# Kernel optimization log

Measured on AMD Instinct MI355X. Metric: run time of the kernel, lower is better.

The kernel has to match this reference:

```python
import jax, jax.numpy as jnp
import numpy as np

DIM = 256
NUM_EXPERTS = 16
EXPERT_HIDDEN = 128
ROUTER_HIDDEN = 64
N_TOKENS = 32768


def setup_inputs() -> dict:
    key = jax.random.key(0)
    ks = jax.random.split(key, 9)
    s = lambda fan_in: 1.0 / np.sqrt(fan_in)
    x = jax.random.normal(ks[0], (N_TOKENS, DIM), dtype=jnp.float32)
    # Router params (Linear(DIM,64) -> ReLU -> Linear(64,E))
    r_w1 = jax.random.uniform(ks[1], (DIM, ROUTER_HIDDEN), jnp.float32, -s(DIM), s(DIM))
    r_b1 = jax.random.uniform(ks[2], (ROUTER_HIDDEN,), jnp.float32, -s(DIM), s(DIM))
    r_w2 = jax.random.uniform(ks[3], (ROUTER_HIDDEN, NUM_EXPERTS), jnp.float32, -s(ROUTER_HIDDEN), s(ROUTER_HIDDEN))
    r_b2 = jax.random.uniform(ks[4], (NUM_EXPERTS,), jnp.float32, -s(ROUTER_HIDDEN), s(ROUTER_HIDDEN))
    # Expert params, stacked over experts: Linear(DIM,128) -> Tanh -> Linear(128,DIM)
    e_w1 = jax.random.uniform(ks[5], (NUM_EXPERTS, DIM, EXPERT_HIDDEN), jnp.float32, -s(DIM), s(DIM))
    e_b1 = jax.random.uniform(ks[6], (NUM_EXPERTS, EXPERT_HIDDEN), jnp.float32, -s(DIM), s(DIM))
    e_w2 = jax.random.uniform(ks[7], (NUM_EXPERTS, EXPERT_HIDDEN, DIM), jnp.float32, -s(EXPERT_HIDDEN), s(EXPERT_HIDDEN))
    e_b2 = jax.random.uniform(ks[8], (NUM_EXPERTS, DIM), jnp.float32, -s(EXPERT_HIDDEN), s(EXPERT_HIDDEN))
    return {"x": x, "r_w1": r_w1, "r_b1": r_b1, "r_w2": r_w2, "r_b2": r_b2,
            "e_w1": e_w1, "e_b1": e_b1, "e_w2": e_w2, "e_b2": e_b2}


def reference(x, r_w1, r_b1, r_w2, r_b2, e_w1, e_b1, e_w2, e_b2):
    # Router: softmax(Linear(ReLU(Linear(x)))), temp=1.0
    h_r = jax.nn.relu(x @ r_w1 + r_b1)                      # [N, 64]
    w = jax.nn.softmax(h_r @ r_w2 + r_b2, axis=-1)          # [N, E]
    # All experts densely (faithful to the reference loop), batched over E.
    h = jnp.tanh(jnp.einsum('nd,edh->neh', x, e_w1) + e_b1[None, :, :])   # [N, E, H]
    outs = jnp.einsum('neh,ehd->ned', h, e_w2) + e_b2[None, :, :]         # [N, E, D]
    # Top-2 gating: mask, renormalize, combine.
    top_val, top_idx = jax.lax.top_k(w, 2)                  # [N, 2]
    n = w.shape[0]
    mask = jnp.zeros_like(w).at[jnp.arange(n)[:, None], top_idx].set(1.0)
    w_top = w * mask
    w_top = w_top / (jnp.sum(w_top, axis=-1, keepdims=True) + 1e-8)
    y_pred = jnp.einsum('ne,ned->nd', w_top, outs)          # [N, D]
    return (y_pred, w)
```

## Files before the change

### kernel.cpp

```cpp
#include <hip/hip_runtime.h>
#include <math.h>

#define NT 32768
#define DIM 256
#define NE 16
#define EH 128
#define RH 64
#define TB 64
#define NPERS 512

#define IB (NT * DIM)
#define WS_COUNTS (IB)
#define WS_OFFSETS (IB + 16)
#define WS_CURSORS (IB + 33)
#define WS_NBLK (IB + 49)
#define WS_TABLE (IB + 64)
#define WS_TOKE (IB + 4096)
#define WS_LIST (WS_TOKE + 2 * NT)
#define WS_TOKG (WS_LIST + 2 * NT)
#define WS_INV (WS_TOKG + 2 * NT)
#define WS_END_I (WS_INV + 2 * NT)
#define U_OUT 0
#define U_W1T (2 * WS_END_I)
#define U_W2T (U_W1T + NE * DIM * EH)
#define U_XG (U_W2T + NE * DIM * EH)

typedef __attribute__((ext_vector_type(4))) float f32x4;
typedef __attribute__((ext_vector_type(8))) short bf16x8;
typedef __attribute__((ext_vector_type(8))) unsigned short us8;

#define SWZ9(b) ((b) ^ (((b) >> 5) & 0x70))
#define SWZ8(b) ((b) ^ (((b) >> 4) & 0x70))

__device__ inline unsigned short f2bf(float f) {
    unsigned int bits = __builtin_bit_cast(unsigned int, f);
    bits += 0x7fffu + ((bits >> 16) & 1u);
    return (unsigned short)(bits >> 16);
}
__device__ inline float bf2f(unsigned short u) {
    unsigned int v = ((unsigned int)u) << 16;
    return __builtin_bit_cast(float, v);
}
__device__ inline float fast_tanh(float v) {
    float cv = fminf(fmaxf(v, -15.f), 15.f);
    float ex = __expf(2.f * cv);
    return (ex - 1.f) / (ex + 1.f);
}

__global__ __launch_bounds__(256) void router_kernel(
    const float* __restrict__ x,
    const float* __restrict__ rw1, const float* __restrict__ rb1,
    const float* __restrict__ rw2, const float* __restrict__ rb2,
    float* __restrict__ w_out, int* __restrict__ wsi, float* __restrict__ wsf)
{
    __shared__ float xT[64][68];
    __shared__ float w1s[64][64];
    __shared__ float hs[64][68];
    __shared__ float ls[64][20];
    __shared__ int scnt[16];

    const int tid = threadIdx.x;
    const int tok0 = blockIdx.x * 64;
    if (tid < 16) scnt[tid] = 0;

    float acc[4][4];
#pragma unroll
    for (int i = 0; i < 4; ++i)
#pragma unroll
        for (int j = 0; j < 4; ++j) acc[i][j] = 0.f;

    const int tt = (tid & 15) * 4;
    const int hh = (tid >> 4) * 4;

    for (int kc = 0; kc < 4; ++kc) {
        __syncthreads();
#pragma unroll
        for (int i = 0; i < 4; ++i) {
            int idx = tid + 256 * i;
            int t = idx >> 4;
            int d4 = (idx & 15) * 4;
            float4 v = *(const float4*)(x + (size_t)(tok0 + t) * DIM + kc * 64 + d4);
            xT[d4 + 0][t] = v.x; xT[d4 + 1][t] = v.y;
            xT[d4 + 2][t] = v.z; xT[d4 + 3][t] = v.w;
        }
#pragma unroll
        for (int i = 0; i < 4; ++i) {
            int idx = tid + 256 * i;
            int d = idx >> 4;
            int h4 = (idx & 15) * 4;
            *(float4*)&w1s[d][h4] = *(const float4*)(rw1 + (size_t)(kc * 64 + d) * RH + h4);
        }
        __syncthreads();
#pragma unroll 8
        for (int d = 0; d < 64; ++d) {
            const float4 xa4 = *(const float4*)&xT[d][tt];
            const float4 wv4 = *(const float4*)&w1s[d][hh];
            const float xa[4] = {xa4.x, xa4.y, xa4.z, xa4.w};
            const float wv[4] = {wv4.x, wv4.y, wv4.z, wv4.w};
#pragma unroll
            for (int i = 0; i < 4; ++i)
#pragma unroll
                for (int j = 0; j < 4; ++j)
                    acc[i][j] = fmaf(xa[i], wv[j], acc[i][j]);
        }
    }
    __syncthreads();
    {
        const float4 b4 = *(const float4*)(rb1 + hh);
        const float b[4] = {b4.x, b4.y, b4.z, b4.w};
#pragma unroll
        for (int i = 0; i < 4; ++i) {
            float4 hv;
            hv.x = fmaxf(acc[i][0] + b[0], 0.f);
            hv.y = fmaxf(acc[i][1] + b[1], 0.f);
            hv.z = fmaxf(acc[i][2] + b[2], 0.f);
            hv.w = fmaxf(acc[i][3] + b[3], 0.f);
            *(float4*)&hs[tt + i][hh] = hv;
        }
    }
    __syncthreads();
    {
        int tok = tid >> 2;
        int e0 = (tid & 3) * 4;
        float l[4] = {0.f, 0.f, 0.f, 0.f};
#pragma unroll 8
        for (int k = 0; k < 64; ++k) {
            float hv = hs[tok][k];
            float4 wv = *(const float4*)(rw2 + k * NE + e0);
            l[0] = fmaf(hv, wv.x, l[0]);
            l[1] = fmaf(hv, wv.y, l[1]);
            l[2] = fmaf(hv, wv.z, l[2]);
            l[3] = fmaf(hv, wv.w, l[3]);
        }
        float4 lb = *(const float4*)(rb2 + e0);
        ls[tok][e0 + 0] = l[0] + lb.x;
        ls[tok][e0 + 1] = l[1] + lb.y;
        ls[tok][e0 + 2] = l[2] + lb.z;
        ls[tok][e0 + 3] = l[3] + lb.w;
    }
    __syncthreads();
    if (tid < 64) {
        const int tok = tid;
        const int gt = tok0 + tok;
        float v[16];
        float m = -1e30f;
#pragma unroll
        for (int e = 0; e < 16; ++e) { v[e] = ls[tok][e]; m = fmaxf(m, v[e]); }
        float s = 0.f;
#pragma unroll
        for (int e = 0; e < 16; ++e) { v[e] = expf(v[e] - m); s += v[e]; }
        const float inv = 1.0f / s;
#pragma unroll
        for (int e = 0; e < 16; ++e) v[e] *= inv;
#pragma unroll
        for (int e = 0; e < 16; e += 4) {
            float4 wv = make_float4(v[e], v[e + 1], v[e + 2], v[e + 3]);
            *(float4*)(w_out + (size_t)gt * NE + e) = wv;
        }
        float v1 = -1.f, v2 = -1.f; int i1 = 0, i2 = 0;
#pragma unroll
        for (int e = 0; e < 16; ++e) {
            if (v[e] > v1) { v2 = v1; i2 = i1; v1 = v[e]; i1 = e; }
            else if (v[e] > v2) { v2 = v[e]; i2 = e; }
        }
        const float den = v1 + v2 + 1e-8f;
        atomicAdd(&scnt[i1], 1);
        atomicAdd(&scnt[i2], 1);
        wsi[WS_TOKE + 2 * gt + 0] = i1;
        wsi[WS_TOKE + 2 * gt + 1] = i2;
        wsf[WS_TOKG + 2 * gt + 0] = v1 / den;
        wsf[WS_TOKG + 2 * gt + 1] = v2 / den;
    }
    __syncthreads();
    if (tid < 16 && scnt[tid]) atomicAdd(&wsi[WS_COUNTS + tid], scnt[tid]);
}

__global__ __launch_bounds__(256) void wprep_kernel(
    const float* __restrict__ ew1, const float* __restrict__ ew2,
    unsigned short* __restrict__ w1t, unsigned short* __restrict__ w2t)
{
    __shared__ float t[64][65];
    int b = blockIdx.x;
    const float* src; unsigned short* dst; int R, C, tr, tc;
    if (b < 128) {
        int e = b >> 3, t8 = b & 7; tr = t8 >> 1; tc = t8 & 1;
        src = ew1 + (size_t)e * DIM * EH; R = DIM; C = EH;
        dst = w1t + (size_t)e * DIM * EH;
    } else {
        int b2 = b - 128; int e = b2 >> 3, t8 = b2 & 7; tr = t8 & 1; tc = t8 >> 1;
        src = ew2 + (size_t)e * EH * DIM; R = EH; C = DIM;
        dst = w2t + (size_t)e * EH * DIM;
    }
    const int R0 = tr * 64, C0 = tc * 64;
    const int tid = threadIdx.x;
#pragma unroll
    for (int q = 0; q < 4; ++q) {
        int r = (tid >> 4) + q * 16, c = (tid & 15) * 4;
        float4 v = *(const float4*)(src + (size_t)(R0 + r) * C + C0 + c);
        t[r][c] = v.x; t[r][c + 1] = v.y; t[r][c + 2] = v.z; t[r][c + 3] = v.w;
    }
    __syncthreads();
#pragma unroll
    for (int q = 0; q < 2; ++q) {
        int rp = (tid >> 3) + q * 32, c0 = (tid & 7) * 8;
        us8 u;
#pragma unroll
        for (int k = 0; k < 8; ++k) u[k] = f2bf(t[c0 + k][rp]);
        *(us8*)(dst + (size_t)(C0 + rp) * R + R0 + c0) = u;
    }
}

__global__ __launch_bounds__(64) void scan_kernel(int* __restrict__ wsi)
{
    __shared__ int soff[17], snc[16];
    const int tid = threadIdx.x;
    if (tid == 0) {
        int off = 0, nb = 0;
        soff[0] = 0;
        for (int e = 0; e < NE; ++e) {
            int c = wsi[WS_COUNTS + e];
            wsi[WS_CURSORS + e] = off;
            wsi[WS_OFFSETS + e] = off;
            off += c;
            soff[e + 1] = off;
            snc[e] = nb;
            nb += (c + TB - 1) / TB;
        }
        wsi[WS_OFFSETS + NE] = off;
        wsi[WS_NBLK] = nb;
    }
    __syncthreads();
    for (int e = 0; e < NE; ++e) {
        int nc = (soff[e + 1] - soff[e] + TB - 1) / TB;
        for (int k = tid; k < nc; k += 64)
            wsi[WS_TABLE + snc[e] + k] = (e << 16) | k;
    }
}

__global__ __launch_bounds__(256) void scatter_kernel(int* __restrict__ wsi)
{
    __shared__ int scnt[16], sbase[16];
    const int tid = threadIdx.x;
    const int t = blockIdx.x * 256 + tid;
    if (tid < 16) scnt[tid] = 0;
    __syncthreads();
    const int e0 = wsi[WS_TOKE + 2 * t + 0];
    const int e1 = wsi[WS_TOKE + 2 * t + 1];
    const int l0 = atomicAdd(&scnt[e0], 1);
    const int l1 = atomicAdd(&scnt[e1], 1);
    __syncthreads();
    if (tid < 16) sbase[tid] = scnt[tid] ? atomicAdd(&wsi[WS_CURSORS + tid], scnt[tid]) : 0;
    __syncthreads();
    const int p0 = sbase[e0] + l0;
    const int p1 = sbase[e1] + l1;
    wsi[WS_LIST + p0] = t;
    wsi[WS_LIST + p1] = t;
    wsi[WS_INV + 2 * t + 0] = p0;
    wsi[WS_INV + 2 * t + 1] = p1;
}

__global__ __launch_bounds__(256) void gather_kernel(
    const float* __restrict__ x, const int* __restrict__ wsi,
    unsigned short* __restrict__ xg)
{
    const int tid = threadIdx.x;
    const int p = blockIdx.x * 32 + (tid >> 3);
    const int sub = tid & 7;
    const int tok = wsi[WS_LIST + p];
    const float* src = x + (size_t)tok * DIM + sub * 32;
    unsigned short* dst = xg + (size_t)p * DIM + sub * 32;
    float4 v[8];
#pragma unroll
    for (int i = 0; i < 8; ++i) v[i] = *(const float4*)(src + i * 4);
#pragma unroll
    for (int i = 0; i < 4; ++i) {
        us8 u;
        u[0] = f2bf(v[2 * i].x);     u[1] = f2bf(v[2 * i].y);
        u[2] = f2bf(v[2 * i].z);     u[3] = f2bf(v[2 * i].w);
        u[4] = f2bf(v[2 * i + 1].x); u[5] = f2bf(v[2 * i + 1].y);
        u[6] = f2bf(v[2 * i + 1].z); u[7] = f2bf(v[2 * i + 1].w);
        *(us8*)(dst + i * 8) = u;
    }
}

__global__ __launch_bounds__(256, 2) void expert_kernel(
    const unsigned short* __restrict__ xg,
    const float* __restrict__ eb1, const float* __restrict__ eb2,
    const unsigned short* __restrict__ w1t, const unsigned short* __restrict__ w2t,
    const int* __restrict__ wsi,
    unsigned short* __restrict__ out_lin)
{
    __shared__ unsigned short smem[16384];
    __shared__ unsigned short obufb[64 * 264];

    const int nblk = wsi[WS_NBLK];
    const int tid = threadIdx.x;
    const int lane = tid & 63, w = tid >> 6;
    const int l15 = lane & 15;
    const int kq = lane >> 4;
    const int q4 = kq * 4;
    char* lds = (char*)smem;
    f32x4 zero4; zero4[0] = zero4[1] = zero4[2] = zero4[3] = 0.f;

    for (int bi = blockIdx.x; bi < nblk; bi += NPERS) {
        const int ent = wsi[WS_TABLE + bi];
        const int e = ent >> 16;
        const int c = ent & 0xffff;
        const int start = wsi[WS_OFFSETS + e] + c * TB;
        const int cnt = min(TB, wsi[WS_OFFSETS + e + 1] - start);

        const char* xrow = (const char*)(xg + (size_t)start * DIM);
        us8 ubuf[8];
#pragma unroll
        for (int i = 0; i < 8; ++i)
            ubuf[i] = *(const us8*)(xrow + (tid + i * 256) * 16);

        const char* w1e = (const char*)(w1t + (size_t)e * DIM * EH);
        bf16x8 b1[8][2];
#pragma unroll
        for (int ks = 0; ks < 8; ++ks)
#pragma unroll
            for (int nt = 0; nt < 2; ++nt)
                b1[ks][nt] = *(const bf16x8*)(w1e + (w * 32 + nt * 16 + l15) * 512 + ks * 64 + kq * 16);

#pragma unroll
        for (int i = 0; i < 8; ++i)
            *(us8*)(lds + SWZ9((tid + i * 256) * 16)) = ubuf[i];
        __syncthreads();

        f32x4 acc[4][2];
#pragma unroll
        for (int i = 0; i < 4; ++i)
#pragma unroll
            for (int j = 0; j < 2; ++j) acc[i][j] = zero4;

#pragma unroll
        for (int ks = 0; ks < 8; ++ks) {
            bf16x8 a[4];
#pragma unroll
            for (int mt = 0; mt < 4; ++mt)
                a[mt] = *(const bf16x8*)(lds + SWZ9((mt * 16 + l15) * 512 + ks * 64 + kq * 16));
#pragma unroll
            for (int mt = 0; mt < 4; ++mt)
#pragma unroll
                for (int nt = 0; nt < 2; ++nt)
                    acc[mt][nt] = __builtin_amdgcn_mfma_f32_16x16x32_bf16(a[mt], b1[ks][nt], acc[mt][nt], 0, 0, 0);
        }

        const char* w2e = (const char*)(w2t + (size_t)e * EH * DIM);
        bf16x8 b2a[4][2];
#pragma unroll
        for (int ks = 0; ks < 4; ++ks)
#pragma unroll
            for (int nt = 0; nt < 2; ++nt)
                b2a[ks][nt] = *(const bf16x8*)(w2e + (w * 64 + nt * 16 + l15) * 256 + ks * 64 + kq * 16);

        __syncthreads();

#pragma unroll
        for (int nt = 0; nt < 2; ++nt) {
            const int h = w * 32 + nt * 16 + l15;
            const float b1v = eb1[e * EH + h];
#pragma unroll
            for (int mt = 0; mt < 4; ++mt)
#pragma unroll
                for (int r = 0; r < 4; ++r) {
                    int tok = mt * 16 + q4 + r;
                    *(unsigned short*)(lds + SWZ8(tok * 256 + h * 2)) = f2bf(fast_tanh(acc[mt][nt][r] + b1v));
                }
        }
        __syncthreads();

        bf16x8 b2b[4][2];
#pragma unroll
        for (int ks = 0; ks < 4; ++ks)
#pragma unroll
            for (int nt = 0; nt < 2; ++nt)
                b2b[ks][nt] = *(const bf16x8*)(w2e + (w * 64 + 32 + nt * 16 + l15) * 256 + ks * 64 + kq * 16);

        {
            f32x4 acc2[4][2];
#pragma unroll
            for (int i = 0; i < 4; ++i)
#pragma unroll
                for (int j = 0; j < 2; ++j) acc2[i][j] = zero4;
#pragma unroll
            for (int ks = 0; ks < 4; ++ks) {
                bf16x8 a[4];
#pragma unroll
                for (int mt = 0; mt < 4; ++mt)
                    a[mt] = *(const bf16x8*)(lds + SWZ8((mt * 16 + l15) * 256 + ks * 64 + kq * 16));
#pragma unroll
                for (int mt = 0; mt < 4; ++mt)
#pragma unroll
                    for (int nt = 0; nt < 2; ++nt)
                        acc2[mt][nt] = __builtin_amdgcn_mfma_f32_16x16x32_bf16(a[mt], b2a[ks][nt], acc2[mt][nt], 0, 0, 0);
            }
            float b2v[2];
#pragma unroll
            for (int nt = 0; nt < 2; ++nt)
                b2v[nt] = eb2[e * DIM + w * 64 + nt * 16 + l15];
#pragma unroll
            for (int mt = 0; mt < 4; ++mt)
#pragma unroll
                for (int nt = 0; nt < 2; ++nt)
#pragma unroll
                    for (int r = 0; r < 4; ++r)
                        obufb[(mt * 16 + q4 + r) * 264 + w * 64 + nt * 16 + l15] =
                            f2bf(acc2[mt][nt][r] + b2v[nt]);
        }
        {
            f32x4 acc2[4][2];
#pragma unroll
            for (int i = 0; i < 4; ++i)
#pragma unroll
                for (int j = 0; j < 2; ++j) acc2[i][j] = zero4;
#pragma unroll
            for (int ks = 0; ks < 4; ++ks) {
                bf16x8 a[4];
#pragma unroll
                for (int mt = 0; mt < 4; ++mt)
                    a[mt] = *(const bf16x8*)(lds + SWZ8((mt * 16 + l15) * 256 + ks * 64 + kq * 16));
#pragma unroll
                for (int mt = 0; mt < 4; ++mt)
#pragma unroll
                    for (int nt = 0; nt < 2; ++nt)
                        acc2[mt][nt] = __builtin_amdgcn_mfma_f32_16x16x32_bf16(a[mt], b2b[ks][nt], acc2[mt][nt], 0, 0, 0);
            }
            float b2v[2];
#pragma unroll
            for (int nt = 0; nt < 2; ++nt)
                b2v[nt] = eb2[e * DIM + w * 64 + 32 + nt * 16 + l15];
#pragma unroll
            for (int mt = 0; mt < 4; ++mt)
#pragma unroll
                for (int nt = 0; nt < 2; ++nt)
#pragma unroll
                    for (int r = 0; r < 4; ++r)
                        obufb[(mt * 16 + q4 + r) * 264 + w * 64 + 32 + nt * 16 + l15] =
                            f2bf(acc2[mt][nt][r] + b2v[nt]);
        }
        __syncthreads();

        {
            const int row = tid >> 2, sub = tid & 3;
            if (row < cnt) {
                const unsigned short* src = obufb + row * 264 + sub * 64;
                unsigned short* dst = out_lin + (size_t)(start + row) * DIM + sub * 64;
#pragma unroll
                for (int i = 0; i < 8; ++i)
                    *(us8*)(dst + i * 8) = *(const us8*)(src + i * 8);
            }
        }
    }
}

__global__ __launch_bounds__(256) void combine_kernel(
    const unsigned short* __restrict__ out_lin,
    const int* __restrict__ wsi, const float* __restrict__ wsf,
    float* __restrict__ y)
{
    const int tid = threadIdx.x;
    const int t = blockIdx.x * 32 + (tid >> 3);
    const int sub = tid & 7;
    const int p0 = wsi[WS_INV + 2 * t + 0];
    const int p1 = wsi[WS_INV + 2 * t + 1];
    const float g0 = wsf[WS_TOKG + 2 * t + 0];
    const float g1 = wsf[WS_TOKG + 2 * t + 1];
    const unsigned short* a = out_lin + (size_t)p0 * DIM + sub * 32;
    const unsigned short* b = out_lin + (size_t)p1 * DIM + sub * 32;
    float* dst = y + (size_t)t * DIM + sub * 32;
    us8 ua[4], ub[4];
#pragma unroll
    for (int i = 0; i < 4; ++i) {
        ua[i] = *(const us8*)(a + i * 8);
        ub[i] = *(const us8*)(b + i * 8);
    }
#pragma unroll
    for (int i = 0; i < 4; ++i) {
        float4 o0, o1;
        o0.x = fmaf(g1, bf2f(ub[i][0]), g0 * bf2f(ua[i][0]));
        o0.y = fmaf(g1, bf2f(ub[i][1]), g0 * bf2f(ua[i][1]));
        o0.z = fmaf(g1, bf2f(ub[i][2]), g0 * bf2f(ua[i][2]));
        o0.w = fmaf(g1, bf2f(ub[i][3]), g0 * bf2f(ua[i][3]));
        o1.x = fmaf(g1, bf2f(ub[i][4]), g0 * bf2f(ua[i][4]));
        o1.y = fmaf(g1, bf2f(ub[i][5]), g0 * bf2f(ua[i][5]));
        o1.z = fmaf(g1, bf2f(ub[i][6]), g0 * bf2f(ua[i][6]));
        o1.w = fmaf(g1, bf2f(ub[i][7]), g0 * bf2f(ua[i][7]));
        *(float4*)(dst + i * 8) = o0;
        *(float4*)(dst + i * 8 + 4) = o1;
    }
}

extern "C" void kernel_launch(void* const* d_in, const int* in_sizes, int n_in,
                              void* d_out, int out_size, void* d_ws, size_t ws_size,
                              hipStream_t stream)
{
    const float* x = (const float*)d_in[0];
    const float* rw1 = (const float*)d_in[1];
    const float* rb1 = (const float*)d_in[2];
    const float* rw2 = (const float*)d_in[3];
    const float* rb2 = (const float*)d_in[4];
    const float* ew1 = (const float*)d_in[5];
    const float* eb1 = (const float*)d_in[6];
    const float* ew2 = (const float*)d_in[7];
    const float* eb2 = (const float*)d_in[8];

    float* y = (float*)d_out;
    float* w_out = y + (size_t)NT * DIM;
    int* wsi = (int*)d_ws;
    float* wsf = (float*)d_ws;
    unsigned short* wsu = (unsigned short*)d_ws;

    hipMemsetAsync(wsi + WS_COUNTS, 0, NE * sizeof(int), stream);

    wprep_kernel<<<256, 256, 0, stream>>>(ew1, ew2, wsu + U_W1T, wsu + U_W2T);
    router_kernel<<<NT / 64, 256, 0, stream>>>(x, rw1, rb1, rw2, rb2, w_out, wsi, wsf);
    scan_kernel<<<1, 64, 0, stream>>>(wsi);
    scatter_kernel<<<NT / 256, 256, 0, stream>>>(wsi);
    gather_kernel<<<2 * NT / 32, 256, 0, stream>>>(x, wsi, wsu + U_XG);
    expert_kernel<<<NPERS, 256, 0, stream>>>(wsu + U_XG, eb1, eb2,
                                             wsu + U_W1T, wsu + U_W2T,
                                             wsi, wsu + U_OUT);
    combine_kernel<<<NT / 32, 256, 0, stream>>>(wsu + U_OUT, wsi, wsf, y);
}
```

Before: 121.3 us.

## Merge weight prep into router kernel and fuse gather into per-wave expert GEMM

Weight transpose/bf16 conversion blocks now run as extra blocks of the router launch, removing a separate kernel. The gather kernel and its bf16 staging buffer are dropped: each wave of the expert kernel handles a 16-token chunk, loads x rows directly from fp32, converts them in registers, and runs both expert GEMMs with weights streamed from global memory instead of LDS-shared tiles. This removes a launch and a full round trip of gathered activations, but each wave reloads the full expert weights for only 16 tokens, which raises weight traffic and L2 pressure.

```diff
diff --git a/kernel.cpp b/kernel.cpp
--- a/kernel.cpp
+++ b/kernel.cpp
@@ -6,8 +6,7 @@
 #define NE 16
 #define EH 128
 #define RH 64
-#define TB 64
-#define NPERS 512
+#define TBE 16
 
 #define IB (NT * DIM)
 #define WS_COUNTS (IB)
@@ -15,7 +14,7 @@
 #define WS_CURSORS (IB + 33)
 #define WS_NBLK (IB + 49)
 #define WS_TABLE (IB + 64)
-#define WS_TOKE (IB + 4096)
+#define WS_TOKE (IB + 8192)
 #define WS_LIST (WS_TOKE + 2 * NT)
 #define WS_TOKG (WS_LIST + 2 * NT)
 #define WS_INV (WS_TOKG + 2 * NT)
@@ -23,14 +22,10 @@
 #define U_OUT 0
 #define U_W1T (2 * WS_END_I)
 #define U_W2T (U_W1T + NE * DIM * EH)
-#define U_XG (U_W2T + NE * DIM * EH)
 
 typedef __attribute__((ext_vector_type(4))) float f32x4;
 typedef __attribute__((ext_vector_type(8))) short bf16x8;
 typedef __attribute__((ext_vector_type(8))) unsigned short us8;
-
-#define SWZ9(b) ((b) ^ (((b) >> 5) & 0x70))
-#define SWZ8(b) ((b) ^ (((b) >> 4) & 0x70))
 
 __device__ inline unsigned short f2bf(float f) {
     unsigned int bits = __builtin_bit_cast(unsigned int, f);
@@ -46,20 +41,59 @@
     float ex = __expf(2.f * cv);
     return (ex - 1.f) / (ex + 1.f);
 }
-
-__global__ __launch_bounds__(256) void router_kernel(
+__device__ inline unsigned int packbf(float a, float b) {
+    return (unsigned int)f2bf(a) | ((unsigned int)f2bf(b) << 16);
+}
+
+__global__ __launch_bounds__(256) void mega_kernel(
     const float* __restrict__ x,
     const float* __restrict__ rw1, const float* __restrict__ rb1,
     const float* __restrict__ rw2, const float* __restrict__ rb2,
-    float* __restrict__ w_out, int* __restrict__ wsi, float* __restrict__ wsf)
-{
-    __shared__ float xT[64][68];
-    __shared__ float w1s[64][64];
-    __shared__ float hs[64][68];
-    __shared__ float ls[64][20];
-    __shared__ int scnt[16];
-
+    const float* __restrict__ ew1, const float* __restrict__ ew2,
+    float* __restrict__ w_out, int* __restrict__ wsi, float* __restrict__ wsf,
+    unsigned short* __restrict__ w1t, unsigned short* __restrict__ w2t)
+{
+    __shared__ char pool[56448];
     const int tid = threadIdx.x;
+
+    if ((int)blockIdx.x >= 512) {
+        float (*t)[65] = (float(*)[65])pool;
+        int b = blockIdx.x - 512;
+        const float* src; unsigned short* dst; int R, C, tr, tc;
+        if (b < 128) {
+            int e = b >> 3, t8 = b & 7; tr = t8 >> 1; tc = t8 & 1;
+            src = ew1 + (size_t)e * DIM * EH; R = DIM; C = EH;
+            dst = w1t + (size_t)e * DIM * EH;
+        } else {
+            int b2 = b - 128; int e = b2 >> 3, t8 = b2 & 7; tr = t8 & 1; tc = t8 >> 1;
+            src = ew2 + (size_t)e * EH * DIM; R = EH; C = DIM;
+            dst = w2t + (size_t)e * EH * DIM;
+        }
+        const int R0 = tr * 64, C0 = tc * 64;
+#pragma unroll
+        for (int q = 0; q < 4; ++q) {
+            int r = (tid >> 4) + q * 16, c = (tid & 15) * 4;
+            float4 v = *(const float4*)(src + (size_t)(R0 + r) * C + C0 + c);
+            t[r][c] = v.x; t[r][c + 1] = v.y; t[r][c + 2] = v.z; t[r][c + 3] = v.w;
+        }
+        __syncthreads();
+#pragma unroll
+        for (int q = 0; q < 2; ++q) {
+            int rp = (tid >> 3) + q * 32, c0 = (tid & 7) * 8;
+            us8 u;
+#pragma unroll
+            for (int k = 0; k < 8; ++k) u[k] = f2bf(t[c0 + k][rp]);
+            *(us8*)(dst + (size_t)(C0 + rp) * R + R0 + c0) = u;
+        }
+        return;
+    }
+
+    float (*xT)[68] = (float(*)[68])pool;
+    float (*w1s)[64] = (float(*)[64])(pool + 17408);
+    float (*hs)[68] = (float(*)[68])(pool + 33792);
+    float (*ls)[20] = (float(*)[20])(pool + 51200);
+    int* scnt = (int*)(pool + 56320);
+
     const int tok0 = blockIdx.x * 64;
     if (tid < 16) scnt[tid] = 0;
 
@@ -77,11 +111,11 @@
 #pragma unroll
         for (int i = 0; i < 4; ++i) {
             int idx = tid + 256 * i;
-            int t = idx >> 4;
+            int t2 = idx >> 4;
             int d4 = (idx & 15) * 4;
-            float4 v = *(const float4*)(x + (size_t)(tok0 + t) * DIM + kc * 64 + d4);
-            xT[d4 + 0][t] = v.x; xT[d4 + 1][t] = v.y;
-            xT[d4 + 2][t] = v.z; xT[d4 + 3][t] = v.w;
+            float4 v = *(const float4*)(x + (size_t)(tok0 + t2) * DIM + kc * 64 + d4);
+            xT[d4 + 0][t2] = v.x; xT[d4 + 1][t2] = v.y;
+            xT[d4 + 2][t2] = v.z; xT[d4 + 3][t2] = v.w;
         }
 #pragma unroll
         for (int i = 0; i < 4; ++i) {
@@ -175,41 +209,6 @@
     if (tid < 16 && scnt[tid]) atomicAdd(&wsi[WS_COUNTS + tid], scnt[tid]);
 }
 
-__global__ __launch_bounds__(256) void wprep_kernel(
-    const float* __restrict__ ew1, const float* __restrict__ ew2,
-    unsigned short* __restrict__ w1t, unsigned short* __restrict__ w2t)
-{
-    __shared__ float t[64][65];
-    int b = blockIdx.x;
-    const float* src; unsigned short* dst; int R, C, tr, tc;
-    if (b < 128) {
-        int e = b >> 3, t8 = b & 7; tr = t8 >> 1; tc = t8 & 1;
-        src = ew1 + (size_t)e * DIM * EH; R = DIM; C = EH;
-        dst = w1t + (size_t)e * DIM * EH;
-    } else {
-        int b2 = b - 128; int e = b2 >> 3, t8 = b2 & 7; tr = t8 & 1; tc = t8 >> 1;
-        src = ew2 + (size_t)e * EH * DIM; R = EH; C = DIM;
-        dst = w2t + (size_t)e * EH * DIM;
-    }
-    const int R0 = tr * 64, C0 = tc * 64;
-    const int tid = threadIdx.x;
-#pragma unroll
-    for (int q = 0; q < 4; ++q) {
-        int r = (tid >> 4) + q * 16, c = (tid & 15) * 4;
-        float4 v = *(const float4*)(src + (size_t)(R0 + r) * C + C0 + c);
-        t[r][c] = v.x; t[r][c + 1] = v.y; t[r][c + 2] = v.z; t[r][c + 3] = v.w;
-    }
-    __syncthreads();
-#pragma unroll
-    for (int q = 0; q < 2; ++q) {
-        int rp = (tid >> 3) + q * 32, c0 = (tid & 7) * 8;
-        us8 u;
-#pragma unroll
-        for (int k = 0; k < 8; ++k) u[k] = f2bf(t[c0 + k][rp]);
-        *(us8*)(dst + (size_t)(C0 + rp) * R + R0 + c0) = u;
-    }
-}
-
 __global__ __launch_bounds__(64) void scan_kernel(int* __restrict__ wsi)
 {
     __shared__ int soff[17], snc[16];
@@ -224,14 +223,14 @@
             off += c;
             soff[e + 1] = off;
             snc[e] = nb;
-            nb += (c + TB - 1) / TB;
+            nb += (c + TBE - 1) / TBE;
         }
         wsi[WS_OFFSETS + NE] = off;
         wsi[WS_NBLK] = nb;
     }
     __syncthreads();
     for (int e = 0; e < NE; ++e) {
-        int nc = (soff[e + 1] - soff[e] + TB - 1) / TB;
+        int nc = (soff[e + 1] - soff[e] + TBE - 1) / TBE;
         for (int k = tid; k < nc; k += 64)
             wsi[WS_TABLE + snc[e] + k] = (e << 16) | k;
     }
@@ -259,199 +258,101 @@
     wsi[WS_INV + 2 * t + 1] = p1;
 }
 
-__global__ __launch_bounds__(256) void gather_kernel(
-    const float* __restrict__ x, const int* __restrict__ wsi,
-    unsigned short* __restrict__ xg)
-{
-    const int tid = threadIdx.x;
-    const int p = blockIdx.x * 32 + (tid >> 3);
-    const int sub = tid & 7;
-    const int tok = wsi[WS_LIST + p];
-    const float* src = x + (size_t)tok * DIM + sub * 32;
-    unsigned short* dst = xg + (size_t)p * DIM + sub * 32;
-    float4 v[8];
-#pragma unroll
-    for (int i = 0; i < 8; ++i) v[i] = *(const float4*)(src + i * 4);
-#pragma unroll
-    for (int i = 0; i < 4; ++i) {
-        us8 u;
-        u[0] = f2bf(v[2 * i].x);     u[1] = f2bf(v[2 * i].y);
-        u[2] = f2bf(v[2 * i].z);     u[3] = f2bf(v[2 * i].w);
-        u[4] = f2bf(v[2 * i + 1].x); u[5] = f2bf(v[2 * i + 1].y);
-        u[6] = f2bf(v[2 * i + 1].z); u[7] = f2bf(v[2 * i + 1].w);
-        *(us8*)(dst + i * 8) = u;
-    }
-}
-
-__global__ __launch_bounds__(256, 2) void expert_kernel(
-    const unsigned short* __restrict__ xg,
+__global__ __launch_bounds__(256, 3) void expert_kernel(
+    const float* __restrict__ x,
     const float* __restrict__ eb1, const float* __restrict__ eb2,
     const unsigned short* __restrict__ w1t, const unsigned short* __restrict__ w2t,
     const int* __restrict__ wsi,
     unsigned short* __restrict__ out_lin)
 {
-    __shared__ unsigned short smem[16384];
-    __shared__ unsigned short obufb[64 * 264];
+    __shared__ char smem[4][8448];
+
+    const int tid = threadIdx.x;
+    const int wave = tid >> 6, lane = tid & 63;
+    const int l15 = lane & 15;
+    const int q = lane >> 4;
 
     const int nblk = wsi[WS_NBLK];
-    const int tid = threadIdx.x;
-    const int lane = tid & 63, w = tid >> 6;
-    const int l15 = lane & 15;
-    const int kq = lane >> 4;
-    const int q4 = kq * 4;
-    char* lds = (char*)smem;
+    const int chunk = blockIdx.x * 4 + wave;
+    if (chunk >= nblk) return;
+
+    const int ent = wsi[WS_TABLE + chunk];
+    const int e = ent >> 16;
+    const int c = ent & 0xffff;
+    const int start = wsi[WS_OFFSETS + e] + c * TBE;
+    const int cnt = min(TBE, wsi[WS_OFFSETS + e + 1] - start);
+
+    const int tok = wsi[WS_LIST + start + (l15 < cnt ? l15 : 0)];
+    char* sl = smem[wave];
+
     f32x4 zero4; zero4[0] = zero4[1] = zero4[2] = zero4[3] = 0.f;
 
-    for (int bi = blockIdx.x; bi < nblk; bi += NPERS) {
-        const int ent = wsi[WS_TABLE + bi];
-        const int e = ent >> 16;
-        const int c = ent & 0xffff;
-        const int start = wsi[WS_OFFSETS + e] + c * TB;
-        const int cnt = min(TB, wsi[WS_OFFSETS + e + 1] - start);
-
-        const char* xrow = (const char*)(xg + (size_t)start * DIM);
-        us8 ubuf[8];
-#pragma unroll
-        for (int i = 0; i < 8; ++i)
-            ubuf[i] = *(const us8*)(xrow + (tid + i * 256) * 16);
-
-        const char* w1e = (const char*)(w1t + (size_t)e * DIM * EH);
-        bf16x8 b1[8][2];
-#pragma unroll
-        for (int ks = 0; ks < 8; ++ks)
-#pragma unroll
-            for (int nt = 0; nt < 2; ++nt)
-                b1[ks][nt] = *(const bf16x8*)(w1e + (w * 32 + nt * 16 + l15) * 512 + ks * 64 + kq * 16);
-
-#pragma unroll
-        for (int i = 0; i < 8; ++i)
-            *(us8*)(lds + SWZ9((tid + i * 256) * 16)) = ubuf[i];
-        __syncthreads();
-
-        f32x4 acc[4][2];
-#pragma unroll
-        for (int i = 0; i < 4; ++i)
-#pragma unroll
-            for (int j = 0; j < 2; ++j) acc[i][j] = zero4;
-
-#pragma unroll
-        for (int ks = 0; ks < 8; ++ks) {
-            bf16x8 a[4];
-#pragma unroll
-            for (int mt = 0; mt < 4; ++mt)
-                a[mt] = *(const bf16x8*)(lds + SWZ9((mt * 16 + l15) * 512 + ks * 64 + kq * 16));
-#pragma unroll
-            for (int mt = 0; mt < 4; ++mt)
-#pragma unroll
-                for (int nt = 0; nt < 2; ++nt)
-                    acc[mt][nt] = __builtin_amdgcn_mfma_f32_16x16x32_bf16(a[mt], b1[ks][nt], acc[mt][nt], 0, 0, 0);
-        }
-
-        const char* w2e = (const char*)(w2t + (size_t)e * EH * DIM);
-        bf16x8 b2a[4][2];
-#pragma unroll
-        for (int ks = 0; ks < 4; ++ks)
-#pragma unroll
-            for (int nt = 0; nt < 2; ++nt)
-                b2a[ks][nt] = *(const bf16x8*)(w2e + (w * 64 + nt * 16 + l15) * 256 + ks * 64 + kq * 16);
-
-        __syncthreads();
-
-#pragma unroll
-        for (int nt = 0; nt < 2; ++nt) {
-            const int h = w * 32 + nt * 16 + l15;
-            const float b1v = eb1[e * EH + h];
-#pragma unroll
-            for (int mt = 0; mt < 4; ++mt)
-#pragma unroll
-                for (int r = 0; r < 4; ++r) {
-                    int tok = mt * 16 + q4 + r;
-                    *(unsigned short*)(lds + SWZ8(tok * 256 + h * 2)) = f2bf(fast_tanh(acc[mt][nt][r] + b1v));
-                }
-        }
-        __syncthreads();
-
-        bf16x8 b2b[4][2];
-#pragma unroll
-        for (int ks = 0; ks < 4; ++ks)
-#pragma unroll
-            for (int nt = 0; nt < 2; ++nt)
-                b2b[ks][nt] = *(const bf16x8*)(w2e + (w * 64 + 32 + nt * 16 + l15) * 256 + ks * 64 + kq * 16);
-
-        {
-            f32x4 acc2[4][2];
-#pragma unroll
-            for (int i = 0; i < 4; ++i)
-#pragma unroll
-                for (int j = 0; j < 2; ++j) acc2[i][j] = zero4;
-#pragma unroll
-            for (int ks = 0; ks < 4; ++ks) {
-                bf16x8 a[4];
-#pragma unroll
-                for (int mt = 0; mt < 4; ++mt)
-                    a[mt] = *(const bf16x8*)(lds + SWZ8((mt * 16 + l15) * 256 + ks * 64 + kq * 16));
-#pragma unroll
-                for (int mt = 0; mt < 4; ++mt)
-#pragma unroll
-                    for (int nt = 0; nt < 2; ++nt)
-                        acc2[mt][nt] = __builtin_amdgcn_mfma_f32_16x16x32_bf16(a[mt], b2a[ks][nt], acc2[mt][nt], 0, 0, 0);
-            }
-            float b2v[2];
-#pragma unroll
-            for (int nt = 0; nt < 2; ++nt)
-                b2v[nt] = eb2[e * DIM + w * 64 + nt * 16 + l15];
-#pragma unroll
-            for (int mt = 0; mt < 4; ++mt)
-#pragma unroll
-                for (int nt = 0; nt < 2; ++nt)
-#pragma unroll
-                    for (int r = 0; r < 4; ++r)
-                        obufb[(mt * 16 + q4 + r) * 264 + w * 64 + nt * 16 + l15] =
-                            f2bf(acc2[mt][nt][r] + b2v[nt]);
-        }
-        {
-            f32x4 acc2[4][2];
-#pragma unroll
-            for (int i = 0; i < 4; ++i)
-#pragma unroll
-                for (int j = 0; j < 2; ++j) acc2[i][j] = zero4;
-#pragma unroll
-            for (int ks = 0; ks < 4; ++ks) {
-                bf16x8 a[4];
-#pragma unroll
-                for (int mt = 0; mt < 4; ++mt)
-                    a[mt] = *(const bf16x8*)(lds + SWZ8((mt * 16 + l15) * 256 + ks * 64 + kq * 16));
-#pragma unroll
-                for (int mt = 0; mt < 4; ++mt)
-#pragma unroll
-                    for (int nt = 0; nt < 2; ++nt)
-                        acc2[mt][nt] = __builtin_amdgcn_mfma_f32_16x16x32_bf16(a[mt], b2b[ks][nt], acc2[mt][nt], 0, 0, 0);
-            }
-            float b2v[2];
-#pragma unroll
-            for (int nt = 0; nt < 2; ++nt)
-                b2v[nt] = eb2[e * DIM + w * 64 + 32 + nt * 16 + l15];
-#pragma unroll
-            for (int mt = 0; mt < 4; ++mt)
-#pragma unroll
-                for (int nt = 0; nt < 2; ++nt)
-#pragma unroll
-                    for (int r = 0; r < 4; ++r)
-                        obufb[(mt * 16 + q4 + r) * 264 + w * 64 + 32 + nt * 16 + l15] =
-                            f2bf(acc2[mt][nt][r] + b2v[nt]);
-        }
-        __syncthreads();
-
-        {
-            const int row = tid >> 2, sub = tid & 3;
-            if (row < cnt) {
-                const unsigned short* src = obufb + row * 264 + sub * 64;
-                unsigned short* dst = out_lin + (size_t)(start + row) * DIM + sub * 64;
-#pragma unroll
-                for (int i = 0; i < 8; ++i)
-                    *(us8*)(dst + i * 8) = *(const us8*)(src + i * 8);
-            }
-        }
+    const float* xr = x + (size_t)tok * DIM;
+    bf16x8 xf[8];
+#pragma unroll
+    for (int ks = 0; ks < 8; ++ks) {
+        float4 a = *(const float4*)(xr + ks * 32 + q * 8);
+        float4 b = *(const float4*)(xr + ks * 32 + q * 8 + 4);
+        bf16x8 u;
+        u[0] = (short)f2bf(a.x); u[1] = (short)f2bf(a.y);
+        u[2] = (short)f2bf(a.z); u[3] = (short)f2bf(a.w);
+        u[4] = (short)f2bf(b.x); u[5] = (short)f2bf(b.y);
+        u[6] = (short)f2bf(b.z); u[7] = (short)f2bf(b.w);
+        xf[ks] = u;
+    }
+
+    const char* w1e = (const char*)(w1t + (size_t)e * DIM * EH);
+    f32x4 acc1[8];
+#pragma unroll
+    for (int i = 0; i < 8; ++i) acc1[i] = zero4;
+#pragma unroll
+    for (int ks = 0; ks < 8; ++ks) {
+        bf16x8 wf[8];
+#pragma unroll
+        for (int nt = 0; nt < 8; ++nt)
+            wf[nt] = *(const bf16x8*)(w1e + (nt * 16 + l15) * 512 + ks * 64 + q * 16);
+#pragma unroll
+        for (int nt = 0; nt < 8; ++nt)
+            acc1[nt] = __builtin_amdgcn_mfma_f32_16x16x32_bf16(wf[nt], xf[ks], acc1[nt], 0, 0, 0);
+    }
+
+#pragma unroll
+    for (int nt = 0; nt < 8; ++nt) {
+        float4 b1v = *(const float4*)(eb1 + e * EH + nt * 16 + q * 4);
+        float t0 = fast_tanh(acc1[nt][0] + b1v.x);
+        float t1 = fast_tanh(acc1[nt][1] + b1v.y);
+        float t2 = fast_tanh(acc1[nt][2] + b1v.z);
+        float t3 = fast_tanh(acc1[nt][3] + b1v.w);
+        *(unsigned int*)(sl + l15 * 260 + nt * 32 + q * 8) = packbf(t0, t1);
+        *(unsigned int*)(sl + l15 * 260 + nt * 32 + q * 8 + 4) = packbf(t2, t3);
+    }
+
+    bf16x8 h2[4];
+#pragma unroll
+    for (int ks2 = 0; ks2 < 4; ++ks2)
+        h2[ks2] = *(const bf16x8*)(sl + l15 * 260 + ks2 * 64 + q * 16);
+
+    const char* w2e = (const char*)(w2t + (size_t)e * EH * DIM);
+#pragma unroll
+    for (int nt = 0; nt < 16; ++nt) {
+        f32x4 a2 = zero4;
+#pragma unroll
+        for (int ks2 = 0; ks2 < 4; ++ks2) {
+            bf16x8 wf = *(const bf16x8*)(w2e + (nt * 16 + l15) * 256 + ks2 * 64 + q * 16);
+            a2 = __builtin_amdgcn_mfma_f32_16x16x32_bf16(wf, h2[ks2], a2, 0, 0, 0);
+        }
+        float4 b2v = *(const float4*)(eb2 + e * DIM + nt * 16 + q * 4);
+        *(unsigned int*)(sl + l15 * 516 + nt * 32 + q * 8) = packbf(a2[0] + b2v.x, a2[1] + b2v.y);
+        *(unsigned int*)(sl + l15 * 516 + nt * 32 + q * 8 + 4) = packbf(a2[2] + b2v.z, a2[3] + b2v.w);
+    }
+
+    char* ob = (char*)out_lin + (size_t)start * 512;
+#pragma unroll
+    for (int k = 0; k < 8; ++k) {
+        int f = k * 1024 + lane * 16;
+        int row = f >> 9, col = f & 511;
+        if (row < cnt)
+            *(us8*)(ob + row * 512 + col) = *(const us8*)(sl + row * 516 + col);
     }
 }
 
@@ -514,13 +415,11 @@
 
     hipMemsetAsync(wsi + WS_COUNTS, 0, NE * sizeof(int), stream);
 
-    wprep_kernel<<<256, 256, 0, stream>>>(ew1, ew2, wsu + U_W1T, wsu + U_W2T);
-    router_kernel<<<NT / 64, 256, 0, stream>>>(x, rw1, rb1, rw2, rb2, w_out, wsi, wsf);
+    mega_kernel<<<768, 256, 0, stream>>>(x, rw1, rb1, rw2, rb2, ew1, ew2,
+                                         w_out, wsi, wsf, wsu + U_W1T, wsu + U_W2T);
     scan_kernel<<<1, 64, 0, stream>>>(wsi);
     scatter_kernel<<<NT / 256, 256, 0, stream>>>(wsi);
-    gather_kernel<<<2 * NT / 32, 256, 0, stream>>>(x, wsi, wsu + U_XG);
-    expert_kernel<<<NPERS, 256, 0, stream>>>(wsu + U_XG, eb1, eb2,
-                                             wsu + U_W1T, wsu + U_W2T,
-                                             wsi, wsu + U_OUT);
+    expert_kernel<<<1028, 256, 0, stream>>>(x, eb1, eb2, wsu + U_W1T, wsu + U_W2T,
+                                            wsi, wsu + U_OUT);
     combine_kernel<<<NT / 32, 256, 0, stream>>>(wsu + U_OUT, wsi, wsf, y);
 }
```

Result: slower. 148.4 us (+22.3%).

## Fuse weight prep into router kernel and prefetch next expert tile activations

Applied to the files above, without the earlier changes.

Merges the weight transpose/bf16 conversion kernel into the router kernel as extra blocks using a shared LDS pool, removing one launch and letting both run concurrently. In the persistent expert kernel, the next tile's table entry and activation rows are loaded into registers while the current tile computes, hiding global load latency. This raises register pressure and LDS usage in the fused kernel.

```diff
diff --git a/kernel.cpp b/kernel.cpp
--- a/kernel.cpp
+++ b/kernel.cpp
@@ -47,19 +47,55 @@
     return (ex - 1.f) / (ex + 1.f);
 }
 
-__global__ __launch_bounds__(256) void router_kernel(
+__global__ __launch_bounds__(256) void mega_kernel(
     const float* __restrict__ x,
     const float* __restrict__ rw1, const float* __restrict__ rb1,
     const float* __restrict__ rw2, const float* __restrict__ rb2,
-    float* __restrict__ w_out, int* __restrict__ wsi, float* __restrict__ wsf)
-{
-    __shared__ float xT[64][68];
-    __shared__ float w1s[64][64];
-    __shared__ float hs[64][68];
-    __shared__ float ls[64][20];
-    __shared__ int scnt[16];
-
+    const float* __restrict__ ew1, const float* __restrict__ ew2,
+    float* __restrict__ w_out, int* __restrict__ wsi, float* __restrict__ wsf,
+    unsigned short* __restrict__ w1t, unsigned short* __restrict__ w2t)
+{
+    __shared__ char pool[56448];
     const int tid = threadIdx.x;
+
+    if ((int)blockIdx.x >= 512) {
+        float (*t)[65] = (float(*)[65])pool;
+        int b = blockIdx.x - 512;
+        const float* src; unsigned short* dst; int R, C, tr, tc;
+        if (b < 128) {
+            int e = b >> 3, t8 = b & 7; tr = t8 >> 1; tc = t8 & 1;
+            src = ew1 + (size_t)e * DIM * EH; R = DIM; C = EH;
+            dst = w1t + (size_t)e * DIM * EH;
+        } else {
+            int b2 = b - 128; int e = b2 >> 3, t8 = b2 & 7; tr = t8 & 1; tc = t8 >> 1;
+            src = ew2 + (size_t)e * EH * DIM; R = EH; C = DIM;
+            dst = w2t + (size_t)e * EH * DIM;
+        }
+        const int R0 = tr * 64, C0 = tc * 64;
+#pragma unroll
+        for (int q = 0; q < 4; ++q) {
+            int r = (tid >> 4) + q * 16, c = (tid & 15) * 4;
+            float4 v = *(const float4*)(src + (size_t)(R0 + r) * C + C0 + c);
+            t[r][c] = v.x; t[r][c + 1] = v.y; t[r][c + 2] = v.z; t[r][c + 3] = v.w;
+        }
+        __syncthreads();
+#pragma unroll
+        for (int q = 0; q < 2; ++q) {
+            int rp = (tid >> 3) + q * 32, c0 = (tid & 7) * 8;
+            us8 u;
+#pragma unroll
+            for (int k = 0; k < 8; ++k) u[k] = f2bf(t[c0 + k][rp]);
+            *(us8*)(dst + (size_t)(C0 + rp) * R + R0 + c0) = u;
+        }
+        return;
+    }
+
+    float (*xT)[68] = (float(*)[68])pool;
+    float (*w1s)[64] = (float(*)[64])(pool + 17408);
+    float (*hs)[68] = (float(*)[68])(pool + 33792);
+    float (*ls)[20] = (float(*)[20])(pool + 51200);
+    int* scnt = (int*)(pool + 56320);
+
     const int tok0 = blockIdx.x * 64;
     if (tid < 16) scnt[tid] = 0;
 
@@ -77,11 +113,11 @@
 #pragma unroll
         for (int i = 0; i < 4; ++i) {
             int idx = tid + 256 * i;
-            int t = idx >> 4;
+            int t2 = idx >> 4;
             int d4 = (idx & 15) * 4;
-            float4 v = *(const float4*)(x + (size_t)(tok0 + t) * DIM + kc * 64 + d4);
-            xT[d4 + 0][t] = v.x; xT[d4 + 1][t] = v.y;
-            xT[d4 + 2][t] = v.z; xT[d4 + 3][t] = v.w;
+            float4 v = *(const float4*)(x + (size_t)(tok0 + t2) * DIM + kc * 64 + d4);
+            xT[d4 + 0][t2] = v.x; xT[d4 + 1][t2] = v.y;
+            xT[d4 + 2][t2] = v.z; xT[d4 + 3][t2] = v.w;
         }
 #pragma unroll
         for (int i = 0; i < 4; ++i) {
@@ -173,41 +209,6 @@
     }
     __syncthreads();
     if (tid < 16 && scnt[tid]) atomicAdd(&wsi[WS_COUNTS + tid], scnt[tid]);
-}
-
-__global__ __launch_bounds__(256) void wprep_kernel(
-    const float* __restrict__ ew1, const float* __restrict__ ew2,
-    unsigned short* __restrict__ w1t, unsigned short* __restrict__ w2t)
-{
-    __shared__ float t[64][65];
-    int b = blockIdx.x;
-    const float* src; unsigned short* dst; int R, C, tr, tc;
-    if (b < 128) {
-        int e = b >> 3, t8 = b & 7; tr = t8 >> 1; tc = t8 & 1;
-        src = ew1 + (size_t)e * DIM * EH; R = DIM; C = EH;
-        dst = w1t + (size_t)e * DIM * EH;
-    } else {
-        int b2 = b - 128; int e = b2 >> 3, t8 = b2 & 7; tr = t8 & 1; tc = t8 >> 1;
-        src = ew2 + (size_t)e * EH * DIM; R = EH; C = DIM;
-        dst = w2t + (size_t)e * EH * DIM;
-    }
-    const int R0 = tr * 64, C0 = tc * 64;
-    const int tid = threadIdx.x;
-#pragma unroll
-    for (int q = 0; q < 4; ++q) {
-        int r = (tid >> 4) + q * 16, c = (tid & 15) * 4;
-        float4 v = *(const float4*)(src + (size_t)(R0 + r) * C + C0 + c);
-        t[r][c] = v.x; t[r][c + 1] = v.y; t[r][c + 2] = v.z; t[r][c + 3] = v.w;
-    }
-    __syncthreads();
-#pragma unroll
-    for (int q = 0; q < 2; ++q) {
-        int rp = (tid >> 3) + q * 32, c0 = (tid & 7) * 8;
-        us8 u;
-#pragma unroll
-        for (int k = 0; k < 8; ++k) u[k] = f2bf(t[c0 + k][rp]);
-        *(us8*)(dst + (size_t)(C0 + rp) * R + R0 + c0) = u;
-    }
 }
 
 __global__ __launch_bounds__(64) void scan_kernel(int* __restrict__ wsi)
@@ -302,18 +303,43 @@
     char* lds = (char*)smem;
     f32x4 zero4; zero4[0] = zero4[1] = zero4[2] = zero4[3] = 0.f;
 
-    for (int bi = blockIdx.x; bi < nblk; bi += NPERS) {
-        const int ent = wsi[WS_TABLE + bi];
-        const int e = ent >> 16;
-        const int c = ent & 0xffff;
-        const int start = wsi[WS_OFFSETS + e] + c * TB;
-        const int cnt = min(TB, wsi[WS_OFFSETS + e + 1] - start);
-
-        const char* xrow = (const char*)(xg + (size_t)start * DIM);
-        us8 ubuf[8];
+    int e_n, start_n, cnt_n;
+    {
+        int ent = wsi[WS_TABLE + blockIdx.x];
+        e_n = ent >> 16;
+        int c = ent & 0xffff;
+        start_n = wsi[WS_OFFSETS + e_n] + c * TB;
+        cnt_n = min(TB, wsi[WS_OFFSETS + e_n + 1] - start_n);
+    }
+    us8 ubuf[8];
+    {
+        const char* xrow = (const char*)(xg + (size_t)start_n * DIM);
 #pragma unroll
         for (int i = 0; i < 8; ++i)
             ubuf[i] = *(const us8*)(xrow + (tid + i * 256) * 16);
+    }
+
+    for (int bi = blockIdx.x; bi < nblk; bi += NPERS) {
+        const int e = e_n, start = start_n, cnt = cnt_n;
+
+#pragma unroll
+        for (int i = 0; i < 8; ++i)
+            *(us8*)(lds + SWZ9((tid + i * 256) * 16)) = ubuf[i];
+
+        {
+            int nbi = bi + NPERS;
+            if (nbi < nblk) {
+                int ent2 = wsi[WS_TABLE + nbi];
+                e_n = ent2 >> 16;
+                int c2 = ent2 & 0xffff;
+                start_n = wsi[WS_OFFSETS + e_n] + c2 * TB;
+                cnt_n = min(TB, wsi[WS_OFFSETS + e_n + 1] - start_n);
+                const char* xrow = (const char*)(xg + (size_t)start_n * DIM);
+#pragma unroll
+                for (int i = 0; i < 8; ++i)
+                    ubuf[i] = *(const us8*)(xrow + (tid + i * 256) * 16);
+            }
+        }
 
         const char* w1e = (const char*)(w1t + (size_t)e * DIM * EH);
         bf16x8 b1[8][2];
@@ -323,9 +349,6 @@
             for (int nt = 0; nt < 2; ++nt)
                 b1[ks][nt] = *(const bf16x8*)(w1e + (w * 32 + nt * 16 + l15) * 512 + ks * 64 + kq * 16);
 
-#pragma unroll
-        for (int i = 0; i < 8; ++i)
-            *(us8*)(lds + SWZ9((tid + i * 256) * 16)) = ubuf[i];
         __syncthreads();
 
         f32x4 acc[4][2];
@@ -514,8 +537,8 @@
 
     hipMemsetAsync(wsi + WS_COUNTS, 0, NE * sizeof(int), stream);
 
-    wprep_kernel<<<256, 256, 0, stream>>>(ew1, ew2, wsu + U_W1T, wsu + U_W2T);
-    router_kernel<<<NT / 64, 256, 0, stream>>>(x, rw1, rb1, rw2, rb2, w_out, wsi, wsf);
+    mega_kernel<<<768, 256, 0, stream>>>(x, rw1, rb1, rw2, rb2, ew1, ew2,
+                                         w_out, wsi, wsf, wsu + U_W1T, wsu + U_W2T);
     scan_kernel<<<1, 64, 0, stream>>>(wsi);
     scatter_kernel<<<NT / 256, 256, 0, stream>>>(wsi);
     gather_kernel<<<2 * NT / 32, 256, 0, stream>>>(x, wsi, wsu + U_XG);
```

New measurement: 125.5 us. 3.4% more time.
